# Kernel optimization log

Measured on AMD Instinct MI355X. Metric: run time of the kernel, lower is better.

Reference implementation:

```python
import jax, jax.numpy as jnp
import numpy as np


def setup_inputs() -> dict:
    key = jax.random.key(0)
    k1, k2, k3, k4, k5 = jax.random.split(key, 5)
    B, H, N, D = 32, 16, 1024, 128  # batch, heads, max_n_codes, head_dim
    transformer_t_1 = jax.random.normal(k1, (B, H, N, D), dtype=jnp.float32)
    transformer_t = jax.random.normal(k2, (B, H, N, D), dtype=jnp.float32)
    # valid-prefix padding vectors: first L entries nonzero, remainder zero
    lengths = jax.random.randint(k3, (B,), N // 2, N + 1)
    padding_t = (jnp.arange(N)[None, :] < lengths[:, None]).astype(jnp.int32)
    concat_w = jax.random.normal(k4, (1, 2 * D), dtype=jnp.float32) / np.sqrt(2 * D)
    concat_b = jax.random.normal(k5, (1,), dtype=jnp.float32) * 0.01
    return {
        "transformer_t_1": transformer_t_1,
        "transformer_t": transformer_t,
        "padding_t": padding_t,
        "max_n_codes": N,
        "concat_w": concat_w,
        "concat_b": concat_b,
    }


def reference(transformer_t_1, transformer_t, padding_t, max_n_codes, concat_w, concat_b):
    N = max_n_codes
    D = transformer_t.shape[-1]
    # create_padding_matrix: padd = index of first zero in padding row (else N);
    # mask positions n >= padd (True = masked out)
    iszero = padding_t == 0                      # [B, N]
    first0 = jnp.argmax(iszero, axis=1)          # [B]
    padd = jnp.where(iszero.any(axis=1), first0, N)
    mask = (jnp.arange(N)[None, :] >= padd[:, None])[:, None, :]  # [B, 1, N] -> bcast over heads

    # all_nodes_t_1: sum over node dim, broadcast back to every node
    s = transformer_t_1.sum(axis=2)              # [B, H, D]
    # concat Linear([all_nodes, transformer_t]) -> split weight into two halves
    w1 = concat_w[0, :D]
    w2 = concat_w[0, D:]
    score = (jnp.einsum('bhd,d->bh', s, w1)[:, :, None]
             + jnp.einsum('bhnd,d->bhn', transformer_t, w2)
             + concat_b[0])                      # [B, H, N]

    logits = jnp.where(mask, -jnp.inf, score)
    attn = jax.nn.softmax(logits, axis=-1)
    attn = jnp.where(mask, jnp.array(0.0, attn.dtype), attn)

    return transformer_t * attn[..., None] + transformer_t
```

## Files before the change

### kernel.cpp

```cpp
#include <hip/hip_runtime.h>

#define BB 32
#define HH 16
#define NN 1024
#define DD 128


#define FOR32(M) M(0) M(1) M(2) M(3) M(4) M(5) M(6) M(7) \
                 M(8) M(9) M(10) M(11) M(12) M(13) M(14) M(15) \
                 M(16) M(17) M(18) M(19) M(20) M(21) M(22) M(23) \
                 M(24) M(25) M(26) M(27) M(28) M(29) M(30) M(31)

#define FORPAIRS(M) M(0,1) M(2,3) M(4,5) M(6,7) M(8,9) M(10,11) M(12,13) \
                    M(14,15) M(16,17) M(18,19) M(20,21) M(22,23) M(24,25) \
                    M(26,27) M(28,29) M(30,31)

__global__ __launch_bounds__(1024, 4) void fused_kernel(const float* __restrict__ t,
                                                        const int* __restrict__ padding,
                                                        const float* __restrict__ w2,
                                                        float* __restrict__ out) {
    const int bh   = blockIdx.x;
    const int b    = bh >> 4;
    const int tid  = threadIdx.x;
    const int wid  = tid >> 6;
    const int lane = tid & 63;

    __shared__ float s_fac[NN];
    __shared__ int   red_i[16];
    __shared__ float red_f[16];

    const float* trow = t + (long)bh * NN * DD;

    int lm = (padding[b * NN + tid] == 0) ? tid : NN;
#pragma unroll
    for (int off = 32; off; off >>= 1) lm = min(lm, __shfl_xor(lm, off));
    if (lane == 0) red_i[wid] = lm;

    const int hw = tid >> 5;
    const int l  = tid & 31;
    const float4 wv = ((const float4*)w2)[l];
    const float4* rowp = (const float4*)(trow + (long)(hw * 32) * DD);

#define DECLV(K) float4 v##K;
    FOR32(DECLV)
#undef DECLV
#define LOADV(K) v##K = rowp[(K) * 32 + l];
    FOR32(LOADV)
#undef LOADV

#define PAIR(K0, K1) {                                                        \
        const float a  = v##K0.x * wv.x + v##K0.y * wv.y                      \
                       + v##K0.z * wv.z + v##K0.w * wv.w;                     \
        const float bq = v##K1.x * wv.x + v##K1.y * wv.y                      \
                       + v##K1.z * wv.z + v##K1.w * wv.w;                     \
        float x = (l < 16) ? a : bq;                                          \
        float y = (l < 16) ? bq : a;                                          \
        x += __shfl_xor(y, 16);                                               \
        x += __shfl_xor(x, 8);                                                \
        x += __shfl_xor(x, 4);                                                \
        x += __shfl_xor(x, 2);                                                \
        x += __shfl_xor(x, 1);                                                \
        const int n = hw * 32 + (K0);                                         \
        if (l == 0)  s_fac[n]     = x;                                        \
        if (l == 16) s_fac[n + 1] = x;                                        \
    }
    FORPAIRS(PAIR)
#undef PAIR

    __syncthreads();

    int padd = NN;
#pragma unroll
    for (int k = 0; k < 16; ++k) padd = min(padd, red_i[k]);

    const float sc  = s_fac[tid];
    const float NEG = -3.4e38f;
    float m = (tid < padd) ? sc : NEG;
#pragma unroll
    for (int off = 32; off; off >>= 1) m = fmaxf(m, __shfl_xor(m, off));
    if (lane == 0) red_f[wid] = m;
    __syncthreads();
    float M = NEG;
#pragma unroll
    for (int k = 0; k < 16; ++k) M = fmaxf(M, red_f[k]);
    __syncthreads();

    const float e = (tid < padd) ? __expf(sc - M) : 0.f;
    float s = e;
#pragma unroll
    for (int off = 32; off; off >>= 1) s += __shfl_xor(s, off);
    if (lane == 0) red_f[wid] = s;
    __syncthreads();
    float S = 0.f;
#pragma unroll
    for (int k = 0; k < 16; ++k) S += red_f[k];

    const float inv = (S > 0.f) ? (1.0f / S) : 0.f;
    s_fac[tid] = 1.f + e * inv;
    __syncthreads();

    float4* o4row = (float4*)(out + (long)bh * NN * DD + (long)(hw * 32) * DD);
#define ST(K) {                                                               \
        const float f = s_fac[hw * 32 + (K)];                                 \
        float4 w = v##K;                                                      \
        w.x *= f; w.y *= f; w.z *= f; w.w *= f;                               \
        o4row[(K) * 32 + l] = w;                                              \
    }
    FOR32(ST)
#undef ST
}

extern "C" void kernel_launch(void* const* d_in, const int* in_sizes, int n_in,
                              void* d_out, int out_size, void* d_ws, size_t ws_size,
                              hipStream_t stream) {
    const float* t       = (const float*)d_in[1];
    const int*   padding = (const int*)d_in[2];
    const float* cw      = (const float*)d_in[4];
    float*       out     = (float*)d_out;

    fused_kernel<<<BB * HH, 1024, 0, stream>>>(t, padding, cw + DD, out);
}
```

Measured before the change: 635.7 us.

## Split each row across four cooperative blocks with cross-block softmax exchange

Replaces the one-block-per-(b,h) 1024-thread kernel with a persistent cooperative grid of 256 blocks of 256 threads. Each block handles a quarter row (256 nodes) per iteration and loops over 8 work items. Blocks publish partial max, sum and padding index through global memory with release/acquire flags and spin until all four quarters arrive, then combine them into a global softmax. This aims to improve occupancy and latency hiding with smaller blocks. In exchange it adds a memset, cooperative launch overhead and inter-block spin synchronization.

```diff
diff --git a/kernel.cpp b/kernel.cpp
--- a/kernel.cpp
+++ b/kernel.cpp
@@ -15,99 +15,138 @@
                     M(14,15) M(16,17) M(18,19) M(20,21) M(22,23) M(24,25) \
                     M(26,27) M(28,29) M(30,31)
 
-__global__ __launch_bounds__(1024, 4) void fused_kernel(const float* __restrict__ t,
-                                                        const int* __restrict__ padding,
-                                                        const float* __restrict__ w2,
-                                                        float* __restrict__ out) {
-    const int bh   = blockIdx.x;
-    const int b    = bh >> 4;
+#define AGENT __HIP_MEMORY_SCOPE_AGENT
+
+__global__ __launch_bounds__(256, 2) void fused_kernel(const float* __restrict__ t,
+                                                       const int* __restrict__ padding,
+                                                       const float* __restrict__ w2,
+                                                       float* __restrict__ out,
+                                                       float* __restrict__ exch,
+                                                       int* __restrict__ flags) {
+    const int j    = blockIdx.x;
     const int tid  = threadIdx.x;
     const int wid  = tid >> 6;
     const int lane = tid & 63;
+    const int hw   = tid >> 5;
+    const int l    = tid & 31;
 
-    __shared__ float s_fac[NN];
-    __shared__ int   red_i[16];
-    __shared__ float red_f[16];
+    __shared__ float s_sc[256];
+    __shared__ float s_fac[256];
+    __shared__ float red_m[4];
+    __shared__ float red_z[4];
+    __shared__ int   red_i[4];
+    __shared__ float s_ex[12];
 
-    const float* trow = t + (long)bh * NN * DD;
+    const float4 wv = ((const float4*)w2)[l];
+    const float  NEG = -3.4e38f;
 
-    int lm = (padding[b * NN + tid] == 0) ? tid : NN;
-#pragma unroll
-    for (int off = 32; off; off >>= 1) lm = min(lm, __shfl_xor(lm, off));
-    if (lane == 0) red_i[wid] = lm;
+    for (int g = 0; g < 8; ++g) {
+        const int q   = g * 256 + j;
+        const int row = q >> 2;
+        const int qi  = q & 3;
+        const int b   = row >> 4;
 
-    const int hw = tid >> 5;
-    const int l  = tid & 31;
-    const float4 wv = ((const float4*)w2)[l];
-    const float4* rowp = (const float4*)(trow + (long)(hw * 32) * DD);
-
+        const float4* base = (const float4*)(t + (long)row * (NN * DD) + (long)qi * (256 * DD));
 #define DECLV(K) float4 v##K;
-    FOR32(DECLV)
+        FOR32(DECLV)
 #undef DECLV
-#define LOADV(K) v##K = rowp[(K) * 32 + l];
-    FOR32(LOADV)
+#define LOADV(K) v##K = base[(K) * 256 + tid];
+        FOR32(LOADV)
 #undef LOADV
 
+        int pl = (padding[b * NN + qi * 256 + tid] == 0) ? tid : 256;
+#pragma unroll
+        for (int off = 32; off; off >>= 1) pl = min(pl, __shfl_xor(pl, off));
+        if (lane == 0) red_i[wid] = pl;
+
 #define PAIR(K0, K1) {                                                        \
-        const float a  = v##K0.x * wv.x + v##K0.y * wv.y                      \
-                       + v##K0.z * wv.z + v##K0.w * wv.w;                     \
-        const float bq = v##K1.x * wv.x + v##K1.y * wv.y                      \
-                       + v##K1.z * wv.z + v##K1.w * wv.w;                     \
-        float x = (l < 16) ? a : bq;                                          \
-        float y = (l < 16) ? bq : a;                                          \
-        x += __shfl_xor(y, 16);                                               \
-        x += __shfl_xor(x, 8);                                                \
-        x += __shfl_xor(x, 4);                                                \
-        x += __shfl_xor(x, 2);                                                \
-        x += __shfl_xor(x, 1);                                                \
-        const int n = hw * 32 + (K0);                                         \
-        if (l == 0)  s_fac[n]     = x;                                        \
-        if (l == 16) s_fac[n + 1] = x;                                        \
+            const float a  = v##K0.x * wv.x + v##K0.y * wv.y                  \
+                           + v##K0.z * wv.z + v##K0.w * wv.w;                 \
+            const float bq = v##K1.x * wv.x + v##K1.y * wv.y                  \
+                           + v##K1.z * wv.z + v##K1.w * wv.w;                 \
+            float x = (l < 16) ? a : bq;                                      \
+            float y = (l < 16) ? bq : a;                                      \
+            x += __shfl_xor(y, 16);                                           \
+            x += __shfl_xor(x, 8);                                            \
+            x += __shfl_xor(x, 4);                                            \
+            x += __shfl_xor(x, 2);                                            \
+            x += __shfl_xor(x, 1);                                            \
+            if (l == 0)  s_sc[(K0) * 8 + hw] = x;                             \
+            if (l == 16) s_sc[(K1) * 8 + hw] = x;                             \
+        }
+        FORPAIRS(PAIR)
+#undef PAIR
+        __syncthreads();
+
+        const int lmin = min(min(red_i[0], red_i[1]), min(red_i[2], red_i[3]));
+
+        const float sc = s_sc[tid];
+        float mm = (tid < lmin) ? sc : NEG;
+#pragma unroll
+        for (int off = 32; off; off >>= 1) mm = fmaxf(mm, __shfl_xor(mm, off));
+        if (lane == 0) red_m[wid] = mm;
+        __syncthreads();
+        const float lm = fmaxf(fmaxf(red_m[0], red_m[1]), fmaxf(red_m[2], red_m[3]));
+
+        const float e = (tid < lmin) ? __expf(sc - lm) : 0.f;
+        float z = e;
+#pragma unroll
+        for (int off = 32; off; off >>= 1) z += __shfl_xor(z, off);
+        if (lane == 0) red_z[wid] = z;
+        __syncthreads();
+        const float lz = red_z[0] + red_z[1] + red_z[2] + red_z[3];
+
+        if (tid == 0) {
+            float* ex = exch + (long)(row * 4 + qi) * 4;
+            __hip_atomic_store(&ex[0], lm, __ATOMIC_RELAXED, AGENT);
+            __hip_atomic_store(&ex[1], lz, __ATOMIC_RELAXED, AGENT);
+            __hip_atomic_store(&ex[2], (float)lmin, __ATOMIC_RELAXED, AGENT);
+            __hip_atomic_fetch_add(&flags[row], 1, __ATOMIC_RELEASE, AGENT);
+            while (__hip_atomic_load(&flags[row], __ATOMIC_ACQUIRE, AGENT) < 4) {
+                __builtin_amdgcn_s_sleep(8);
+            }
+        }
+        __syncthreads();
+
+        if (tid < 12) {
+            const int qq = tid / 3, w = tid % 3;
+            s_ex[tid] = __hip_atomic_load(exch + (long)(row * 4 + qq) * 4 + w,
+                                          __ATOMIC_RELAXED, AGENT);
+        }
+        __syncthreads();
+
+        int padd = NN;
+#pragma unroll
+        for (int qq = 0; qq < 4; ++qq) {
+            const int lq = (int)s_ex[qq * 3 + 2];
+            if (lq < 256) { padd = min(padd, qq * 256 + lq); }
+        }
+        float M = NEG;
+#pragma unroll
+        for (int qq = 0; qq < 4; ++qq)
+            if (qq * 256 < padd) M = fmaxf(M, s_ex[qq * 3 + 0]);
+        float S = 0.f;
+#pragma unroll
+        for (int qq = 0; qq < 4; ++qq)
+            if (qq * 256 < padd) S += s_ex[qq * 3 + 1] * __expf(s_ex[qq * 3 + 0] - M);
+
+        float f = 1.f;
+        if (qi * 256 + tid < padd && S > 0.f)
+            f = 1.f + (e * __expf(lm - M)) / S;
+        s_fac[tid] = f;
+        __syncthreads();
+
+        float4* obase = (float4*)(out + (long)row * (NN * DD) + (long)qi * (256 * DD));
+#define ST(K) {                                                               \
+            const float ff = s_fac[(K) * 8 + hw];                             \
+            float4 w = v##K;                                                  \
+            w.x *= ff; w.y *= ff; w.z *= ff; w.w *= ff;                       \
+            obase[(K) * 256 + tid] = w;                                       \
+        }
+        FOR32(ST)
+#undef ST
+        __syncthreads();
     }
-    FORPAIRS(PAIR)
-#undef PAIR
-
-    __syncthreads();
-
-    int padd = NN;
-#pragma unroll
-    for (int k = 0; k < 16; ++k) padd = min(padd, red_i[k]);
-
-    const float sc  = s_fac[tid];
-    const float NEG = -3.4e38f;
-    float m = (tid < padd) ? sc : NEG;
-#pragma unroll
-    for (int off = 32; off; off >>= 1) m = fmaxf(m, __shfl_xor(m, off));
-    if (lane == 0) red_f[wid] = m;
-    __syncthreads();
-    float M = NEG;
-#pragma unroll
-    for (int k = 0; k < 16; ++k) M = fmaxf(M, red_f[k]);
-    __syncthreads();
-
-    const float e = (tid < padd) ? __expf(sc - M) : 0.f;
-    float s = e;
-#pragma unroll
-    for (int off = 32; off; off >>= 1) s += __shfl_xor(s, off);
-    if (lane == 0) red_f[wid] = s;
-    __syncthreads();
-    float S = 0.f;
-#pragma unroll
-    for (int k = 0; k < 16; ++k) S += red_f[k];
-
-    const float inv = (S > 0.f) ? (1.0f / S) : 0.f;
-    s_fac[tid] = 1.f + e * inv;
-    __syncthreads();
-
-    float4* o4row = (float4*)(out + (long)bh * NN * DD + (long)(hw * 32) * DD);
-#define ST(K) {                                                               \
-        const float f = s_fac[hw * 32 + (K)];                                 \
-        float4 w = v##K;                                                      \
-        w.x *= f; w.y *= f; w.z *= f; w.w *= f;                               \
-        o4row[(K) * 32 + l] = w;                                              \
-    }
-    FOR32(ST)
-#undef ST
 }
 
 extern "C" void kernel_launch(void* const* d_in, const int* in_sizes, int n_in,
@@ -115,8 +154,15 @@
                               hipStream_t stream) {
     const float* t       = (const float*)d_in[1];
     const int*   padding = (const int*)d_in[2];
-    const float* cw      = (const float*)d_in[4];
+    const float* w2p     = (const float*)d_in[4] + DD;
     float*       out     = (float*)d_out;
+    float*       exch    = (float*)d_ws;
+    int*         flags   = (int*)((char*)d_ws + 512 * 4 * 4 * sizeof(float));
 
-    fused_kernel<<<BB * HH, 1024, 0, stream>>>(t, padding, cw + DD, out);
+    hipMemsetAsync(d_ws, 0, 512 * 4 * 4 * sizeof(float) + 512 * sizeof(int), stream);
+
+    void* args[] = { (void*)&t, (void*)&padding, (void*)&w2p, (void*)&out,
+                     (void*)&exch, (void*)&flags };
+    hipLaunchCooperativeKernel((const void*)fused_kernel, dim3(256), dim3(256),
+                               args, 0, stream);
 }
```

Result: no change. 638.7 us (+0.5%).
